# Kernel optimization log

Measured on AMD Instinct MI355X. Metric: run time of the kernel, lower is better.

The kernel has to match this reference:

```python
import jax, jax.numpy as jnp
import numpy as np

HEADS = 8
DIM = 512
SCALE = (DIM // HEADS) ** (-0.5)  # 0.125


def setup_inputs() -> dict:
    key = jax.random.key(0)
    k1, k2, k3, k4 = jax.random.split(key, 4)
    B, C, H, W = 4, DIM, 96, 96
    x = jax.random.normal(k1, (B, C, H, W), dtype=jnp.float32)
    # 1x1 conv weights collapsed to matrices [out_ch, in_ch]
    w_qkv = jax.random.normal(k2, (3 * DIM, DIM), dtype=jnp.float32) * (DIM ** -0.5)
    w_out = jax.random.normal(k3, (DIM, DIM), dtype=jnp.float32) * (DIM ** -0.5)
    b_out = jax.random.normal(k4, (DIM,), dtype=jnp.float32) * 0.01
    return {"x": x, "w_qkv": w_qkv, "w_out": w_out, "b_out": b_out}


def reference(x, w_qkv, w_out, b_out):
    # axis='height' branch of the original forward
    b, c, h, w = x.shape
    heads = HEADS
    d = c // heads
    # 1x1 conv == per-pixel GEMM: [B,3C,H,W]
    qkv = jnp.einsum('bchw,oc->bohw', x, w_qkv)
    # 'b (qkv heads d) x y -> qkv b heads x y d'
    qkv = qkv.reshape(b, 3, heads, d, h, w)
    qkv = jnp.transpose(qkv, (1, 0, 2, 4, 5, 3))  # [3, b, heads, h, w, d]
    q, k, v = qkv[0], qkv[1], qkv[2]
    # attention along the width axis, batched over (b, heads, row x)
    dots = jnp.einsum('bhxid,bhxjd->bhxij', q, k) * SCALE
    attn = jax.nn.softmax(dots, axis=-1)
    out = jnp.einsum('bhxij,bhxjd->bhxid', attn, v)  # [b, heads, h, w, d]
    # 'b heads x y d -> b (heads d) x y'
    out = jnp.transpose(out, (0, 1, 4, 2, 3)).reshape(b, heads * d, h, w)
    # to_out 1x1 conv with bias
    out = jnp.einsum('bchw,oc->bohw', out, w_out) + b_out[None, :, None, None]
    return out
```

## Files before the change

### kernel.cpp

```cpp
#include <hip/hip_runtime.h>

typedef unsigned short u16;
typedef unsigned int u32;
typedef __attribute__((ext_vector_type(8))) short short8;
typedef __attribute__((ext_vector_type(4))) float floatx4;

#define HEADS 8
#define DIM 512
#define HH 96
#define WW 96
#define NPIX 9216
#define M_TOT 36864
#define N_QKV 1536
#define SCALE 0.125f

__device__ __forceinline__ float b2f(u16 v){
    union{float f;u32 u;}x; x.u=((u32)v)<<16; return x.f;
}
__device__ __forceinline__ u16 f2b(float f){
    union{float f;u32 u;}x; x.f=f;
    u32 u=x.u + 0x7fffu + ((x.u>>16)&1u);
    return (u16)(u>>16);
}
__device__ __forceinline__ u32 pack2(float a,float b){
    return (u32)f2b(a) | ((u32)f2b(b)<<16);
}

__device__ __forceinline__ void gload16(const u16* g, u16* l){
    __builtin_amdgcn_global_load_lds(
        (const __attribute__((address_space(1))) u32*)g,
        (__attribute__((address_space(3))) u32*)l, 16, 0, 0);
}

__global__ void detect_dtype(const u16* __restrict__ wq, int* __restrict__ flag){
    __shared__ int cnt;
    if (threadIdx.x==0) cnt=0;
    __syncthreads();
    u16 u = wq[2*threadIdx.x];
    int e = (u>>7)&0xff;
    if (e>=100 && e<=128) atomicAdd(&cnt,1);
    __syncthreads();
    if (threadIdx.x==0) *flag = (cnt>128)?1:0;
}

__global__ __launch_bounds__(256)
void convert_w(const void* __restrict__ wq, const void* __restrict__ wo,
               const int* __restrict__ flag, u16* __restrict__ wqb, u16* __restrict__ wob){
    const int isb = *flag;
    int i = blockIdx.x*256 + threadIdx.x;
    const int nq = N_QKV*DIM;
    if (i < nq){
        wqb[i] = isb ? ((const u16*)wq)[i] : f2b(((const float*)wq)[i]);
    } else {
        int j = i - nq;
        wob[j] = isb ? ((const u16*)wo)[j] : f2b(((const float*)wo)[j]);
    }
}

__global__ __launch_bounds__(256)
void convert_x(const void* __restrict__ xv, const int* __restrict__ flag,
               u16* __restrict__ xb){
    __shared__ u16 tile[64][65];
    const int isb = *flag;
    const int p0 = blockIdx.x*64, c0 = blockIdx.y*64, b = blockIdx.z;
    const int t = threadIdx.x;
    const int pl = t&63, c4 = t>>6;
    const float* x32 = (const float*)xv;
    const u16*   x16 = (const u16*)xv;
    size_t src = ((size_t)b*DIM + c0 + c4)*NPIX + p0 + pl;
    #pragma unroll
    for (int i=0;i<16;i++){
        int cl = c4 + i*4;
        size_t s = src + (size_t)i*4*NPIX;
        tile[cl][pl] = isb ? x16[s] : f2b(x32[s]);
    }
    __syncthreads();
    const int cu = t&31, r8 = t>>5;
    u32* xb32 = (u32*)xb;
    #pragma unroll
    for (int i=0;i<8;i++){
        int pr = r8 + i*8;
        u32 v = (u32)tile[2*cu][pr] | ((u32)tile[2*cu+1][pr]<<16);
        xb32[((size_t)b*NPIX + p0 + pr)*(DIM/2) + (c0>>1) + cu] = v;
    }
}

__global__ __launch_bounds__(512, 2)
void gemm_qkv(const u16* __restrict__ A, const u16* __restrict__ B,
              u16* __restrict__ Cqk, u16* __restrict__ vt){
    __shared__ __align__(16) union ShMem {
        u16 tiles[65536];
        float ctQ[8][16][68];
        float ctV[8][16][132];
    } sh;
    u16* lds = sh.tiles;
    const int id = blockIdx.x;
    const int xcd = id & 7, slot = id >> 3;
    const int q6 = slot/6;
    const int by = xcd*18 + q6;
    const int bx = slot - q6*6;
    const int t = threadIdx.x;
    const int w = t>>6, l = t&63, lr = l&15, lq = l>>4;
    const int wm2 = w>>2, wn4 = w&3;
    const int m0 = by*256, n0 = bx*256;
    const u16* gA0 = A + (size_t)(m0 +       w*16 + lr)*DIM + lq*8;
    const u16* gA1 = A + (size_t)(m0 + 128 + w*16 + lr)*DIM + lq*8;
    const u16* gB0 = B + (size_t)(n0 +       w*16 + lr)*DIM + lq*8;
    const u16* gB1 = B + (size_t)(n0 + 128 + w*16 + lr)*DIM + lq*8;

#define STG(gp, opb, h, ko, bb) do { \
        const u16* _g = (gp) + (ko); \
        u16* _l = lds + (bb)*32768 + (opb) + ((h)*8 + w)*1024; \
        gload16(_g,      _l); \
        gload16(_g + 32, _l + 512); \
    } while(0)

    floatx4 acc[8][4] = {};
    STG(gA0, 0,     0, 0, 0);
    STG(gA1, 0,     1, 0, 0);
    STG(gB0, 16384, 0, 0, 0);
    STG(gB1, 16384, 1, 0, 0);

    #pragma unroll 1
    for (int ktile=0; ktile<8; ++ktile){
        const int cur = ktile&1, nxt = cur^1;
        const int ko = (ktile+1)*64;
        if (ktile < 7){
            STG(gA0, 0, 0, ko, nxt);
            asm volatile("s_waitcnt vmcnt(2)" ::: "memory");
        } else {
            asm volatile("s_waitcnt vmcnt(0)" ::: "memory");
        }
        __builtin_amdgcn_s_barrier();
        asm volatile("" ::: "memory");
        const u16* bA = lds + cur*32768 +         wm2*8192 + l*8;
        const u16* bB = lds + cur*32768 + 16384 + wn4*4096 + l*8;
        short8 af[4][2], bf[2][2];
        #pragma unroll
        for (int mi=0;mi<4;mi++){
            af[mi][0] = *(const short8*)(bA + mi*1024);
            af[mi][1] = *(const short8*)(bA + mi*1024 + 512);
        }
        #pragma unroll
        for (int ni=0;ni<2;ni++){
            bf[ni][0] = *(const short8*)(bB + ni*1024);
            bf[ni][1] = *(const short8*)(bB + ni*1024 + 512);
        }
        if (ktile < 7) STG(gA1, 0, 1, ko, nxt);
        __builtin_amdgcn_s_setprio(1);
        #pragma unroll
        for (int mi=0;mi<4;mi++)
            #pragma unroll
            for (int ni=0;ni<2;ni++){
                acc[mi][ni] = __builtin_amdgcn_mfma_f32_16x16x32_bf16(af[mi][0], bf[ni][0], acc[mi][ni], 0,0,0);
                acc[mi][ni] = __builtin_amdgcn_mfma_f32_16x16x32_bf16(af[mi][1], bf[ni][1], acc[mi][ni], 0,0,0);
            }
        __builtin_amdgcn_s_setprio(0);
        #pragma unroll
        for (int ni=0;ni<2;ni++){
            bf[ni][0] = *(const short8*)(bB + (2+ni)*1024);
            bf[ni][1] = *(const short8*)(bB + (2+ni)*1024 + 512);
        }
        if (ktile < 7) STG(gB0, 16384, 0, ko, nxt);
        __builtin_amdgcn_s_setprio(1);
        #pragma unroll
        for (int mi=0;mi<4;mi++)
            #pragma unroll
            for (int ni=0;ni<2;ni++){
                acc[mi][2+ni] = __builtin_amdgcn_mfma_f32_16x16x32_bf16(af[mi][0], bf[ni][0], acc[mi][2+ni], 0,0,0);
                acc[mi][2+ni] = __builtin_amdgcn_mfma_f32_16x16x32_bf16(af[mi][1], bf[ni][1], acc[mi][2+ni], 0,0,0);
            }
        __builtin_amdgcn_s_setprio(0);
        #pragma unroll
        for (int mi=0;mi<4;mi++){
            af[mi][0] = *(const short8*)(bA + (4+mi)*1024);
            af[mi][1] = *(const short8*)(bA + (4+mi)*1024 + 512);
        }
        if (ktile < 7) STG(gB1, 16384, 1, ko, nxt);
        __builtin_amdgcn_s_setprio(1);
        #pragma unroll
        for (int mi=0;mi<4;mi++)
            #pragma unroll
            for (int ni=0;ni<2;ni++){
                acc[4+mi][2+ni] = __builtin_amdgcn_mfma_f32_16x16x32_bf16(af[mi][0], bf[ni][0], acc[4+mi][2+ni], 0,0,0);
                acc[4+mi][2+ni] = __builtin_amdgcn_mfma_f32_16x16x32_bf16(af[mi][1], bf[ni][1], acc[4+mi][2+ni], 0,0,0);
            }
        __builtin_amdgcn_s_setprio(0);
        #pragma unroll
        for (int ni=0;ni<2;ni++){
            bf[ni][0] = *(const short8*)(bB + ni*1024);
            bf[ni][1] = *(const short8*)(bB + ni*1024 + 512);
        }
        __builtin_amdgcn_s_setprio(1);
        #pragma unroll
        for (int mi=0;mi<4;mi++)
            #pragma unroll
            for (int ni=0;ni<2;ni++){
                acc[4+mi][ni] = __builtin_amdgcn_mfma_f32_16x16x32_bf16(af[mi][0], bf[ni][0], acc[4+mi][ni], 0,0,0);
                acc[4+mi][ni] = __builtin_amdgcn_mfma_f32_16x16x32_bf16(af[mi][1], bf[ni][1], acc[4+mi][ni], 0,0,0);
            }
        __builtin_amdgcn_s_setprio(0);
        asm volatile("" ::: "memory");
        __builtin_amdgcn_s_barrier();
        asm volatile("" ::: "memory");
    }
#undef STG
    if (bx < 4){
        float (*ct)[68] = sh.ctQ[w];
        const int row = l>>2, cg = l&3;
        u16* dstbase = Cqk + (size_t)(m0 + wm2*128)*1024 + n0 + wn4*64 + cg*16;
        #pragma unroll
        for (int mi=0;mi<8;mi++){
            #pragma unroll
            for (int ni=0;ni<4;ni++)
                #pragma unroll
                for (int r=0;r<4;r++)
                    ct[lq*4+r][ni*16+lr] = acc[mi][ni][r];
            const float* cp = &ct[row][cg*16];
            float4 v0 = *(const float4*)(cp);
            float4 v1 = *(const float4*)(cp+4);
            float4 v2 = *(const float4*)(cp+8);
            float4 v3 = *(const float4*)(cp+12);
            uint4 s0, s1;
            s0.x=pack2(v0.x,v0.y); s0.y=pack2(v0.z,v0.w);
            s0.z=pack2(v1.x,v1.y); s0.w=pack2(v1.z,v1.w);
            s1.x=pack2(v2.x,v2.y); s1.y=pack2(v2.z,v2.w);
            s1.z=pack2(v3.x,v3.y); s1.w=pack2(v3.z,v3.w);
            u16* dst = dstbase + (size_t)(mi*16 + row)*1024;
            *((uint4*)dst)     = s0;
            *((uint4*)(dst+8)) = s1;
        }
    } else {
        float (*ct)[132] = sh.ctV[w];
        const int bat  = m0 / NPIX;
        const int pixb = m0 - bat*NPIX + wm2*128;
        const int nl = l>>2, seg = l&3;
        for (int ni=0; ni<4; ni++){
            #pragma unroll
            for (int mi=0;mi<8;mi++)
                #pragma unroll
                for (int r=0;r<4;r++)
                    ct[lr][mi*16 + lq*4 + r] = acc[mi][ni][r];
            int ch  = n0 + wn4*64 + ni*16 + nl - 1024;
            int bh2 = bat*8 + (ch>>6);
            int dd  = ch & 63;
            const float* cp = &ct[nl][seg*32];
            float4 v0 = *(const float4*)(cp);
            float4 v1 = *(const float4*)(cp+4);
            float4 v2 = *(const float4*)(cp+8);
            float4 v3 = *(const float4*)(cp+12);
            float4 v4 = *(const float4*)(cp+16);
            float4 v5 = *(const float4*)(cp+20);
            float4 v6 = *(const float4*)(cp+24);
            float4 v7 = *(const float4*)(cp+28);
            uint4 s0, s1, s2, s3;
            s0.x=pack2(v0.x,v0.y); s0.y=pack2(v0.z,v0.w);
            s0.z=pack2(v1.x,v1.y); s0.w=pack2(v1.z,v1.w);
            s1.x=pack2(v2.x,v2.y); s1.y=pack2(v2.z,v2.w);
            s1.z=pack2(v3.x,v3.y); s1.w=pack2(v3.z,v3.w);
            s2.x=pack2(v4.x,v4.y); s2.y=pack2(v4.z,v4.w);
            s2.z=pack2(v5.x,v5.y); s2.w=pack2(v5.z,v5.w);
            s3.x=pack2(v6.x,v6.y); s3.y=pack2(v6.z,v6.w);
            s3.z=pack2(v7.x,v7.y); s3.w=pack2(v7.z,v7.w);
            u16* dst = vt + (size_t)(bh2*64+dd)*NPIX + pixb + seg*32;
            *((uint4*)dst)      = s0;
            *((uint4*)(dst+8))  = s1;
            *((uint4*)(dst+16)) = s2;
            *((uint4*)(dst+24)) = s3;
        }
    }
}

__global__ __launch_bounds__(256)
void attn_kernel(const u16* __restrict__ qk, const u16* __restrict__ vt,
                 u16* __restrict__ attno){
    __shared__ __align__(16) u16 Qf[6144];
    __shared__ __align__(16) u16 Pb[9984];
    __shared__ float Ss[96][97];
    __shared__ float smax[96][2], ssum[96][2], rinv[96];
    const int t = threadIdx.x;
    const int w = t>>6, l = t&63, lr = l&15, lq = l>>4;
    const int wm = w&1, wn = w>>1;
    const int blk = blockIdx.x;
    const int row  = blk % HH;
    const int bh   = blk / HH;
    const int head = bh & 7;
    const int bat  = bh >> 3;
    const size_t pixrow = (size_t)bat*NPIX + row*WW;
    const u16* qbase = qk + pixrow*1024 + head*64;
    #pragma unroll
    for (int i=0;i<6;i++){
        int c  = w*6 + i;
        int c2 = (c<12) ? c : (c-12);
        int mt = c2>>1, ks = c2&1;
        const u16* g = qbase + (size_t)(mt*16+lr)*1024 + ks*32 + lq*8 + ((c<12)?0:512);
        u16* dst = ((c<12)?Qf:Pb) + c2*512 + l*8;
        gload16(g, dst);
    }
    __syncthreads();
    {
        floatx4 acc[3][3] = {};
        #pragma unroll
        for (int ks=0;ks<2;ks++){
            short8 af[3], bf[3];
            #pragma unroll
            for (int i=0;i<3;i++) af[i] = *(const short8*)&Qf[((wm*3+i)*2+ks)*512 + l*8];
            #pragma unroll
            for (int j=0;j<3;j++) bf[j] = *(const short8*)&Pb[((wn*3+j)*2+ks)*512 + l*8];
            #pragma unroll
            for (int i=0;i<3;i++)
                #pragma unroll
                for (int j=0;j<3;j++)
                    acc[i][j] = __builtin_amdgcn_mfma_f32_16x16x32_bf16(af[i], bf[j], acc[i][j], 0,0,0);
        }
        #pragma unroll
        for (int i=0;i<3;i++)
            #pragma unroll
            for (int j=0;j<3;j++)
                #pragma unroll
                for (int r=0;r<4;r++)
                    Ss[(wm*3+i)*16 + lq*4 + r][(wn*3+j)*16 + lr] = acc[i][j][r]*SCALE;
    }
    __syncthreads();
    #pragma unroll
    for (int i=0;i<3;i++){
        const u16* g = vt + (size_t)(bh*64 + w*16 + lr)*NPIX + row*WW + i*32 + lq*8;
        gload16(g, Qf + (w*3+i)*512 + l*8);
    }
    const int srow = t>>1, shalf = t&1, sbase = shalf*48;
    if (t < 192){
        float m = -1e30f;
        #pragma unroll 8
        for (int j=0;j<48;j++) m = fmaxf(m, Ss[srow][sbase+j]);
        smax[srow][shalf] = m;
    }
    __syncthreads();
    if (t < 192){
        float m2 = fmaxf(smax[srow][0], smax[srow][1]);
        float s = 0.f;
        u32* prow = (u32*)&Pb[srow*104 + sbase];
        #pragma unroll 8
        for (int j=0;j<48;j+=2){
            float e0 = __expf(Ss[srow][sbase+j]   - m2);
            float e1 = __expf(Ss[srow][sbase+j+1] - m2);
            prow[j>>1] = pack2(e0, e1);
            s += e0 + e1;
        }
        ssum[srow][shalf] = s;
    }
    __syncthreads();
    if (t < 192 && shalf==0) rinv[srow] = 1.f/(ssum[srow][0]+ssum[srow][1]);
    floatx4 o[3][2] = {};
    #pragma unroll
    for (int ks2=0;ks2<3;ks2++){
        short8 bf2[2];
        #pragma unroll
        for (int bb=0;bb<2;bb++)
            bf2[bb] = *(const short8*)&Qf[((wn*2+bb)*3+ks2)*512 + l*8];
        #pragma unroll
        for (int aa=0;aa<3;aa++){
            short8 af = *(const short8*)&Pb[((wm*3+aa)*16+lr)*104 + ks2*32 + lq*8];
            #pragma unroll
            for (int bb=0;bb<2;bb++)
                o[aa][bb] = __builtin_amdgcn_mfma_f32_16x16x32_bf16(af, bf2[bb], o[aa][bb], 0,0,0);
        }
    }
    __syncthreads();
    #pragma unroll
    for (int aa=0;aa<3;aa++){
        #pragma unroll
        for (int r=0;r<4;r++){
            int m = (wm*3+aa)*16 + lq*4 + r;
            float rv = rinv[m];
            int d0 = wn*32 + lr;
            Pb[m*72 + d0]      = f2b(o[aa][0][r]*rv);
            Pb[m*72 + d0 + 16] = f2b(o[aa][1][r]*rv);
        }
    }
    __syncthreads();
    #pragma unroll
    for (int i=0;i<3;i++){
        int idx = i*256 + t;
        int rr = idx>>3, seg = idx&7;
        uint4 vv = *(const uint4*)&Pb[rr*72 + seg*8];
        *(uint4*)(attno + (pixrow+rr)*512 + head*64 + seg*8) = vv;
    }
}

__global__ __launch_bounds__(512, 2)
void gemm_out(const u16* __restrict__ A, const u16* __restrict__ B,
              const void* __restrict__ bias, const int* __restrict__ flag,
              void* __restrict__ outv){
    __shared__ __align__(16) union ShMem {
        u16 tiles[65536];
        float ctV[8][16][132];
    } sh;
    u16* lds = sh.tiles;
    const int id = blockIdx.x;
    const int xcd = id & 7, slot = id >> 3;
    const int by = xcd*18 + (slot>>1);
    const int bx = slot & 1;
    const int t = threadIdx.x;
    const int w = t>>6, l = t&63, lr = l&15, lq = l>>4;
    const int wm2 = w>>2, wn4 = w&3;
    const int m0 = by*256, n0 = bx*256;
    const u16* gA0 = A + (size_t)(m0 +       w*16 + lr)*DIM + lq*8;
    const u16* gA1 = A + (size_t)(m0 + 128 + w*16 + lr)*DIM + lq*8;
    const u16* gB0 = B + (size_t)(n0 +       w*16 + lr)*DIM + lq*8;
    const u16* gB1 = B + (size_t)(n0 + 128 + w*16 + lr)*DIM + lq*8;

#define STG(gp, opb, h, ko, bb) do { \
        const u16* _g = (gp) + (ko); \
        u16* _l = lds + (bb)*32768 + (opb) + ((h)*8 + w)*1024; \
        gload16(_g,      _l); \
        gload16(_g + 32, _l + 512); \
    } while(0)

    floatx4 acc[8][4] = {};
    STG(gA0, 0,     0, 0, 0);
    STG(gA1, 0,     1, 0, 0);
    STG(gB0, 16384, 0, 0, 0);
    STG(gB1, 16384, 1, 0, 0);

    #pragma unroll 1
    for (int ktile=0; ktile<8; ++ktile){
        const int cur = ktile&1, nxt = cur^1;
        const int ko = (ktile+1)*64;
        if (ktile < 7){
            STG(gA0, 0, 0, ko, nxt);
            asm volatile("s_waitcnt vmcnt(2)" ::: "memory");
        } else {
            asm volatile("s_waitcnt vmcnt(0)" ::: "memory");
        }
        __builtin_amdgcn_s_barrier();
        asm volatile("" ::: "memory");
        const u16* bA = lds + cur*32768 +         wm2*8192 + l*8;
        const u16* bB = lds + cur*32768 + 16384 + wn4*4096 + l*8;
        short8 af[4][2], bf[2][2];
        #pragma unroll
        for (int mi=0;mi<4;mi++){
            af[mi][0] = *(const short8*)(bA + mi*1024);
            af[mi][1] = *(const short8*)(bA + mi*1024 + 512);
        }
        #pragma unroll
        for (int ni=0;ni<2;ni++){
            bf[ni][0] = *(const short8*)(bB + ni*1024);
            bf[ni][1] = *(const short8*)(bB + ni*1024 + 512);
        }
        if (ktile < 7) STG(gA1, 0, 1, ko, nxt);
        __builtin_amdgcn_s_setprio(1);
        #pragma unroll
        for (int mi=0;mi<4;mi++)
            #pragma unroll
            for (int ni=0;ni<2;ni++){
                acc[mi][ni] = __builtin_amdgcn_mfma_f32_16x16x32_bf16(af[mi][0], bf[ni][0], acc[mi][ni], 0,0,0);
                acc[mi][ni] = __builtin_amdgcn_mfma_f32_16x16x32_bf16(af[mi][1], bf[ni][1], acc[mi][ni], 0,0,0);
            }
        __builtin_amdgcn_s_setprio(0);
        #pragma unroll
        for (int ni=0;ni<2;ni++){
            bf[ni][0] = *(const short8*)(bB + (2+ni)*1024);
            bf[ni][1] = *(const short8*)(bB + (2+ni)*1024 + 512);
        }
        if (ktile < 7) STG(gB0, 16384, 0, ko, nxt);
        __builtin_amdgcn_s_setprio(1);
        #pragma unroll
        for (int mi=0;mi<4;mi++)
            #pragma unroll
            for (int ni=0;ni<2;ni++){
                acc[mi][2+ni] = __builtin_amdgcn_mfma_f32_16x16x32_bf16(af[mi][0], bf[ni][0], acc[mi][2+ni], 0,0,0);
                acc[mi][2+ni] = __builtin_amdgcn_mfma_f32_16x16x32_bf16(af[mi][1], bf[ni][1], acc[mi][2+ni], 0,0,0);
            }
        __builtin_amdgcn_s_setprio(0);
        #pragma unroll
        for (int mi=0;mi<4;mi++){
            af[mi][0] = *(const short8*)(bA + (4+mi)*1024);
            af[mi][1] = *(const short8*)(bA + (4+mi)*1024 + 512);
        }
        if (ktile < 7) STG(gB1, 16384, 1, ko, nxt);
        __builtin_amdgcn_s_setprio(1);
        #pragma unroll
        for (int mi=0;mi<4;mi++)
            #pragma unroll
            for (int ni=0;ni<2;ni++){
                acc[4+mi][2+ni] = __builtin_amdgcn_mfma_f32_16x16x32_bf16(af[mi][0], bf[ni][0], acc[4+mi][2+ni], 0,0,0);
                acc[4+mi][2+ni] = __builtin_amdgcn_mfma_f32_16x16x32_bf16(af[mi][1], bf[ni][1], acc[4+mi][2+ni], 0,0,0);
            }
        __builtin_amdgcn_s_setprio(0);
        #pragma unroll
        for (int ni=0;ni<2;ni++){
            bf[ni][0] = *(const short8*)(bB + ni*1024);
            bf[ni][1] = *(const short8*)(bB + ni*1024 + 512);
        }
        __builtin_amdgcn_s_setprio(1);
        #pragma unroll
        for (int mi=0;mi<4;mi++)
            #pragma unroll
            for (int ni=0;ni<2;ni++){
                acc[4+mi][ni] = __builtin_amdgcn_mfma_f32_16x16x32_bf16(af[mi][0], bf[ni][0], acc[4+mi][ni], 0,0,0);
                acc[4+mi][ni] = __builtin_amdgcn_mfma_f32_16x16x32_bf16(af[mi][1], bf[ni][1], acc[4+mi][ni], 0,0,0);
            }
        __builtin_amdgcn_s_setprio(0);
        asm volatile("" ::: "memory");
        __builtin_amdgcn_s_barrier();
        asm volatile("" ::: "memory");
    }
#undef STG
    const int isb = *flag;
    const int bat  = m0 / NPIX;
    const int pix0 = m0 - bat*NPIX + wm2*128;
    float (*ct)[132] = sh.ctV[w];
    const u16*   b16 = (const u16*)bias;
    const float* b32 = (const float*)bias;
    const int nl = l>>3, seg8 = l&7;
    for (int ni=0; ni<4; ni++){
        #pragma unroll
        for (int mi=0;mi<8;mi++)
            #pragma unroll
            for (int r=0;r<4;r++)
                ct[lr][mi*16 + lq*4 + r] = acc[mi][ni][r];
        #pragma unroll
        for (int p=0;p<2;p++){
            int nrow = nl + p*8;
            int ng = n0 + wn4*64 + ni*16 + nrow;
            float bv = isb ? b2f(b16[ng]) : b32[ng];
            const float* cp = &ct[nrow][seg8*16];
            float4 v0 = *(const float4*)(cp);
            float4 v1 = *(const float4*)(cp+4);
            float4 v2 = *(const float4*)(cp+8);
            float4 v3 = *(const float4*)(cp+12);
            v0.x+=bv; v0.y+=bv; v0.z+=bv; v0.w+=bv;
            v1.x+=bv; v1.y+=bv; v1.z+=bv; v1.w+=bv;
            v2.x+=bv; v2.y+=bv; v2.z+=bv; v2.w+=bv;
            v3.x+=bv; v3.y+=bv; v3.z+=bv; v3.w+=bv;
            size_t off = ((size_t)(bat*DIM + ng))*NPIX + pix0 + seg8*16;
            if (isb){
                uint4 s0, s1;
                s0.x=pack2(v0.x,v0.y); s0.y=pack2(v0.z,v0.w);
                s0.z=pack2(v1.x,v1.y); s0.w=pack2(v1.z,v1.w);
                s1.x=pack2(v2.x,v2.y); s1.y=pack2(v2.z,v2.w);
                s1.z=pack2(v3.x,v3.y); s1.w=pack2(v3.z,v3.w);
                *(uint4*)((u16*)outv + off)     = s0;
                *(uint4*)((u16*)outv + off + 8) = s1;
            } else {
                float* of = (float*)outv + off;
                *(float4*)(of)    = v0;
                *(float4*)(of+4)  = v1;
                *(float4*)(of+8)  = v2;
                *(float4*)(of+12) = v3;
            }
        }
    }
}

extern "C" void kernel_launch(void* const* d_in, const int* in_sizes, int n_in,
                              void* d_out, int out_size, void* d_ws, size_t ws_size,
                              hipStream_t stream){
    const void* x    = d_in[0];
    const void* wqkv = d_in[1];
    const void* wout = d_in[2];
    const void* bout = d_in[3];
    char* wsb = (char*)d_ws;
    int* flag    = (int*)wsb;
    u16* xb      = (u16*)(wsb + 256);
    u16* attn_ws = xb;
    u16* wqb     = xb + (size_t)M_TOT*DIM;
    u16* wob     = wqb + (size_t)N_QKV*DIM;
    u16* qk_ws   = wob + (size_t)DIM*DIM;
    u16* vt_ws   = qk_ws + (size_t)M_TOT*1024;
    detect_dtype<<<1, 256, 0, stream>>>((const u16*)wqkv, flag);
    convert_w<<<4096, 256, 0, stream>>>(wqkv, wout, flag, wqb, wob);
    convert_x<<<dim3(144, 8, 4), 256, 0, stream>>>(x, flag, xb);
    gemm_qkv<<<864, 512, 0, stream>>>(xb, wqb, qk_ws, vt_ws);
    attn_kernel<<<3072, 256, 0, stream>>>(qk_ws, vt_ws, attn_ws);
    gemm_out<<<288, 512, 0, stream>>>(attn_ws, wob, bout, flag, d_out);
}
```

Baseline: 347.2 us.

## Retile QKV and output GEMMs to 256x128 tiles with 4 waves, K-step 32

Both GEMM kernels go from 512-thread blocks with 256x256 output tiles and K-step 64 to 256-thread blocks with 256x128 tiles and K-step 32. LDS use drops from 128KB to 48KB, which doubles the number of blocks and should let more resident blocks overlap loads with MFMA. Each wave still computes a 128x64 sub-tile. The cost is more B-operand traffic per output, and twice as many barriers per K sweep. Separately, the bf16 pack helper now uses the hardware v_cvt_pk_bf16_f32 instruction in place of manual rounding.

```diff
diff --git a/kernel.cpp b/kernel.cpp
--- a/kernel.cpp
+++ b/kernel.cpp
@@ -23,7 +23,8 @@
     return (u16)(u>>16);
 }
 __device__ __forceinline__ u32 pack2(float a,float b){
-    return (u32)f2b(a) | ((u32)f2b(b)<<16);
+    u32 r; asm("v_cvt_pk_bf16_f32 %0, %1, %2" : "=v"(r) : "v"(a), "v"(b));
+    return r;
 }
 
 __device__ __forceinline__ void gload16(const u16* g, u16* l){
@@ -85,130 +86,100 @@
     }
 }
 
-__global__ __launch_bounds__(512, 2)
+__global__ __launch_bounds__(256, 2)
 void gemm_qkv(const u16* __restrict__ A, const u16* __restrict__ B,
               u16* __restrict__ Cqk, u16* __restrict__ vt){
     __shared__ __align__(16) union ShMem {
-        u16 tiles[65536];
-        float ctQ[8][16][68];
-        float ctV[8][16][132];
+        u16 tiles[24576];
+        float ctQ[4][16][68];
+        float ctV[4][16][132];
     } sh;
     u16* lds = sh.tiles;
     const int id = blockIdx.x;
     const int xcd = id & 7, slot = id >> 3;
-    const int q6 = slot/6;
-    const int by = xcd*18 + q6;
-    const int bx = slot - q6*6;
+    const int q12 = slot/12;
+    const int by = xcd*18 + q12;
+    const int bx = slot - q12*12;
     const int t = threadIdx.x;
     const int w = t>>6, l = t&63, lr = l&15, lq = l>>4;
-    const int wm2 = w>>2, wn4 = w&3;
-    const int m0 = by*256, n0 = bx*256;
-    const u16* gA0 = A + (size_t)(m0 +       w*16 + lr)*DIM + lq*8;
-    const u16* gA1 = A + (size_t)(m0 + 128 + w*16 + lr)*DIM + lq*8;
-    const u16* gB0 = B + (size_t)(n0 +       w*16 + lr)*DIM + lq*8;
-    const u16* gB1 = B + (size_t)(n0 + 128 + w*16 + lr)*DIM + lq*8;
-
-#define STG(gp, opb, h, ko, bb) do { \
-        const u16* _g = (gp) + (ko); \
-        u16* _l = lds + (bb)*32768 + (opb) + ((h)*8 + w)*1024; \
-        gload16(_g,      _l); \
-        gload16(_g + 32, _l + 512); \
-    } while(0)
+    const int wm2 = w>>1, wn2 = w&1;
+    const int m0 = by*256, n0 = bx*128;
+    const u16* gA = A + (size_t)(m0 + w*16 + lr)*DIM + lq*8;
+    const u16* gB = B + (size_t)(n0 + w*16 + lr)*DIM + lq*8;
+
+#define STG_A(h, ko, bb) gload16(gA + (size_t)(h)*32768 + (ko), \
+                                 lds + (bb)*12288 + ((h)*4 + w)*512)
+#define STG_B(h, ko, bb) gload16(gB + (size_t)(h)*32768 + (ko), \
+                                 lds + (bb)*12288 + 8192 + ((h)*4 + w)*512)
 
     floatx4 acc[8][4] = {};
-    STG(gA0, 0,     0, 0, 0);
-    STG(gA1, 0,     1, 0, 0);
-    STG(gB0, 16384, 0, 0, 0);
-    STG(gB1, 16384, 1, 0, 0);
+    STG_A(0,0,0); STG_A(1,0,0); STG_A(2,0,0); STG_A(3,0,0);
+    STG_B(0,0,0); STG_B(1,0,0);
 
     #pragma unroll 1
-    for (int ktile=0; ktile<8; ++ktile){
-        const int cur = ktile&1, nxt = cur^1;
-        const int ko = (ktile+1)*64;
-        if (ktile < 7){
-            STG(gA0, 0, 0, ko, nxt);
-            asm volatile("s_waitcnt vmcnt(2)" ::: "memory");
+    for (int kt=0; kt<16; ++kt){
+        const int cur = kt&1, nxt = cur^1;
+        const int ko = (kt+1)*32;
+        if (kt < 15){
+            STG_A(0, ko, nxt);
+            asm volatile("s_waitcnt vmcnt(1)" ::: "memory");
         } else {
             asm volatile("s_waitcnt vmcnt(0)" ::: "memory");
         }
         __builtin_amdgcn_s_barrier();
         asm volatile("" ::: "memory");
-        const u16* bA = lds + cur*32768 +         wm2*8192 + l*8;
-        const u16* bB = lds + cur*32768 + 16384 + wn4*4096 + l*8;
-        short8 af[4][2], bf[2][2];
-        #pragma unroll
-        for (int mi=0;mi<4;mi++){
-            af[mi][0] = *(const short8*)(bA + mi*1024);
-            af[mi][1] = *(const short8*)(bA + mi*1024 + 512);
-        }
-        #pragma unroll
-        for (int ni=0;ni<2;ni++){
-            bf[ni][0] = *(const short8*)(bB + ni*1024);
-            bf[ni][1] = *(const short8*)(bB + ni*1024 + 512);
-        }
-        if (ktile < 7) STG(gA1, 0, 1, ko, nxt);
-        __builtin_amdgcn_s_setprio(1);
-        #pragma unroll
-        for (int mi=0;mi<4;mi++)
-            #pragma unroll
-            for (int ni=0;ni<2;ni++){
-                acc[mi][ni] = __builtin_amdgcn_mfma_f32_16x16x32_bf16(af[mi][0], bf[ni][0], acc[mi][ni], 0,0,0);
-                acc[mi][ni] = __builtin_amdgcn_mfma_f32_16x16x32_bf16(af[mi][1], bf[ni][1], acc[mi][ni], 0,0,0);
-            }
-        __builtin_amdgcn_s_setprio(0);
-        #pragma unroll
-        for (int ni=0;ni<2;ni++){
-            bf[ni][0] = *(const short8*)(bB + (2+ni)*1024);
-            bf[ni][1] = *(const short8*)(bB + (2+ni)*1024 + 512);
-        }
-        if (ktile < 7) STG(gB0, 16384, 0, ko, nxt);
-        __builtin_amdgcn_s_setprio(1);
-        #pragma unroll
-        for (int mi=0;mi<4;mi++)
-            #pragma unroll
-            for (int ni=0;ni<2;ni++){
-                acc[mi][2+ni] = __builtin_amdgcn_mfma_f32_16x16x32_bf16(af[mi][0], bf[ni][0], acc[mi][2+ni], 0,0,0);
-                acc[mi][2+ni] = __builtin_amdgcn_mfma_f32_16x16x32_bf16(af[mi][1], bf[ni][1], acc[mi][2+ni], 0,0,0);
-            }
-        __builtin_amdgcn_s_setprio(0);
-        #pragma unroll
-        for (int mi=0;mi<4;mi++){
-            af[mi][0] = *(const short8*)(bA + (4+mi)*1024);
-            af[mi][1] = *(const short8*)(bA + (4+mi)*1024 + 512);
-        }
-        if (ktile < 7) STG(gB1, 16384, 1, ko, nxt);
-        __builtin_amdgcn_s_setprio(1);
-        #pragma unroll
-        for (int mi=0;mi<4;mi++)
-            #pragma unroll
-            for (int ni=0;ni<2;ni++){
-                acc[4+mi][2+ni] = __builtin_amdgcn_mfma_f32_16x16x32_bf16(af[mi][0], bf[ni][0], acc[4+mi][2+ni], 0,0,0);
-                acc[4+mi][2+ni] = __builtin_amdgcn_mfma_f32_16x16x32_bf16(af[mi][1], bf[ni][1], acc[4+mi][2+ni], 0,0,0);
-            }
-        __builtin_amdgcn_s_setprio(0);
-        #pragma unroll
-        for (int ni=0;ni<2;ni++){
-            bf[ni][0] = *(const short8*)(bB + ni*1024);
-            bf[ni][1] = *(const short8*)(bB + ni*1024 + 512);
-        }
-        __builtin_amdgcn_s_setprio(1);
-        #pragma unroll
-        for (int mi=0;mi<4;mi++)
-            #pragma unroll
-            for (int ni=0;ni<2;ni++){
-                acc[4+mi][ni] = __builtin_amdgcn_mfma_f32_16x16x32_bf16(af[mi][0], bf[ni][0], acc[4+mi][ni], 0,0,0);
-                acc[4+mi][ni] = __builtin_amdgcn_mfma_f32_16x16x32_bf16(af[mi][1], bf[ni][1], acc[4+mi][ni], 0,0,0);
-            }
+        const u16* bA = lds + cur*12288 +        wm2*4096 + l*8;
+        const u16* bB = lds + cur*12288 + 8192 + wn2*2048 + l*8;
+        short8 af[4], blo[2], bhi[2];
+        #pragma unroll
+        for (int mi=0;mi<4;mi++) af[mi] = *(const short8*)(bA + mi*512);
+        blo[0] = *(const short8*)(bB);
+        blo[1] = *(const short8*)(bB + 512);
+        if (kt < 15){ STG_A(1, ko, nxt); STG_A(2, ko, nxt); }
+        __builtin_amdgcn_s_setprio(1);
+        #pragma unroll
+        for (int mi=0;mi<4;mi++){
+            acc[mi][0] = __builtin_amdgcn_mfma_f32_16x16x32_bf16(af[mi], blo[0], acc[mi][0], 0,0,0);
+            acc[mi][1] = __builtin_amdgcn_mfma_f32_16x16x32_bf16(af[mi], blo[1], acc[mi][1], 0,0,0);
+        }
+        __builtin_amdgcn_s_setprio(0);
+        bhi[0] = *(const short8*)(bB + 1024);
+        bhi[1] = *(const short8*)(bB + 1536);
+        if (kt < 15){ STG_A(3, ko, nxt); STG_B(0, ko, nxt); }
+        __builtin_amdgcn_s_setprio(1);
+        #pragma unroll
+        for (int mi=0;mi<4;mi++){
+            acc[mi][2] = __builtin_amdgcn_mfma_f32_16x16x32_bf16(af[mi], bhi[0], acc[mi][2], 0,0,0);
+            acc[mi][3] = __builtin_amdgcn_mfma_f32_16x16x32_bf16(af[mi], bhi[1], acc[mi][3], 0,0,0);
+        }
+        __builtin_amdgcn_s_setprio(0);
+        #pragma unroll
+        for (int mi=0;mi<4;mi++) af[mi] = *(const short8*)(bA + 2048 + mi*512);
+        if (kt < 15){ STG_B(1, ko, nxt); }
+        __builtin_amdgcn_s_setprio(1);
+        #pragma unroll
+        for (int mi=0;mi<4;mi++){
+            acc[4+mi][2] = __builtin_amdgcn_mfma_f32_16x16x32_bf16(af[mi], bhi[0], acc[4+mi][2], 0,0,0);
+            acc[4+mi][3] = __builtin_amdgcn_mfma_f32_16x16x32_bf16(af[mi], bhi[1], acc[4+mi][3], 0,0,0);
+        }
+        __builtin_amdgcn_s_setprio(0);
+        __builtin_amdgcn_s_setprio(1);
+        #pragma unroll
+        for (int mi=0;mi<4;mi++){
+            acc[4+mi][0] = __builtin_amdgcn_mfma_f32_16x16x32_bf16(af[mi], blo[0], acc[4+mi][0], 0,0,0);
+            acc[4+mi][1] = __builtin_amdgcn_mfma_f32_16x16x32_bf16(af[mi], blo[1], acc[4+mi][1], 0,0,0);
+        }
         __builtin_amdgcn_s_setprio(0);
         asm volatile("" ::: "memory");
         __builtin_amdgcn_s_barrier();
         asm volatile("" ::: "memory");
     }
-#undef STG
-    if (bx < 4){
+#undef STG_A
+#undef STG_B
+    if (bx < 8){
         float (*ct)[68] = sh.ctQ[w];
         const int row = l>>2, cg = l&3;
-        u16* dstbase = Cqk + (size_t)(m0 + wm2*128)*1024 + n0 + wn4*64 + cg*16;
+        u16* dstbase = Cqk + (size_t)(m0 + wm2*128)*1024 + n0 + wn2*64 + cg*16;
         #pragma unroll
         for (int mi=0;mi<8;mi++){
             #pragma unroll
@@ -241,7 +212,7 @@
                 #pragma unroll
                 for (int r=0;r<4;r++)
                     ct[lr][mi*16 + lq*4 + r] = acc[mi][ni][r];
-            int ch  = n0 + wn4*64 + ni*16 + nl - 1024;
+            int ch  = n0 + wn2*64 + ni*16 + nl - 1024;
             int bh2 = bat*8 + (ch>>6);
             int dd  = ch & 63;
             const float* cp = &ct[nl][seg*32];
@@ -387,125 +358,95 @@
     }
 }
 
-__global__ __launch_bounds__(512, 2)
+__global__ __launch_bounds__(256, 2)
 void gemm_out(const u16* __restrict__ A, const u16* __restrict__ B,
               const void* __restrict__ bias, const int* __restrict__ flag,
               void* __restrict__ outv){
     __shared__ __align__(16) union ShMem {
-        u16 tiles[65536];
-        float ctV[8][16][132];
+        u16 tiles[24576];
+        float ctV[4][16][132];
     } sh;
     u16* lds = sh.tiles;
     const int id = blockIdx.x;
     const int xcd = id & 7, slot = id >> 3;
-    const int by = xcd*18 + (slot>>1);
-    const int bx = slot & 1;
+    const int by = xcd*18 + (slot>>2);
+    const int bx = slot & 3;
     const int t = threadIdx.x;
     const int w = t>>6, l = t&63, lr = l&15, lq = l>>4;
-    const int wm2 = w>>2, wn4 = w&3;
-    const int m0 = by*256, n0 = bx*256;
-    const u16* gA0 = A + (size_t)(m0 +       w*16 + lr)*DIM + lq*8;
-    const u16* gA1 = A + (size_t)(m0 + 128 + w*16 + lr)*DIM + lq*8;
-    const u16* gB0 = B + (size_t)(n0 +       w*16 + lr)*DIM + lq*8;
-    const u16* gB1 = B + (size_t)(n0 + 128 + w*16 + lr)*DIM + lq*8;
-
-#define STG(gp, opb, h, ko, bb) do { \
-        const u16* _g = (gp) + (ko); \
-        u16* _l = lds + (bb)*32768 + (opb) + ((h)*8 + w)*1024; \
-        gload16(_g,      _l); \
-        gload16(_g + 32, _l + 512); \
-    } while(0)
+    const int wm2 = w>>1, wn2 = w&1;
+    const int m0 = by*256, n0 = bx*128;
+    const u16* gA = A + (size_t)(m0 + w*16 + lr)*DIM + lq*8;
+    const u16* gB = B + (size_t)(n0 + w*16 + lr)*DIM + lq*8;
+
+#define STG_A(h, ko, bb) gload16(gA + (size_t)(h)*32768 + (ko), \
+                                 lds + (bb)*12288 + ((h)*4 + w)*512)
+#define STG_B(h, ko, bb) gload16(gB + (size_t)(h)*32768 + (ko), \
+                                 lds + (bb)*12288 + 8192 + ((h)*4 + w)*512)
 
     floatx4 acc[8][4] = {};
-    STG(gA0, 0,     0, 0, 0);
-    STG(gA1, 0,     1, 0, 0);
-    STG(gB0, 16384, 0, 0, 0);
-    STG(gB1, 16384, 1, 0, 0);
+    STG_A(0,0,0); STG_A(1,0,0); STG_A(2,0,0); STG_A(3,0,0);
+    STG_B(0,0,0); STG_B(1,0,0);
 
     #pragma unroll 1
-    for (int ktile=0; ktile<8; ++ktile){
-        const int cur = ktile&1, nxt = cur^1;
-        const int ko = (ktile+1)*64;
-        if (ktile < 7){
-            STG(gA0, 0, 0, ko, nxt);
-            asm volatile("s_waitcnt vmcnt(2)" ::: "memory");
+    for (int kt=0; kt<16; ++kt){
+        const int cur = kt&1, nxt = cur^1;
+        const int ko = (kt+1)*32;
+        if (kt < 15){
+            STG_A(0, ko, nxt);
+            asm volatile("s_waitcnt vmcnt(1)" ::: "memory");
         } else {
             asm volatile("s_waitcnt vmcnt(0)" ::: "memory");
         }
         __builtin_amdgcn_s_barrier();
         asm volatile("" ::: "memory");
-        const u16* bA = lds + cur*32768 +         wm2*8192 + l*8;
-        const u16* bB = lds + cur*32768 + 16384 + wn4*4096 + l*8;
-        short8 af[4][2], bf[2][2];
-        #pragma unroll
-        for (int mi=0;mi<4;mi++){
-            af[mi][0] = *(const short8*)(bA + mi*1024);
-            af[mi][1] = *(const short8*)(bA + mi*1024 + 512);
-        }
-        #pragma unroll
-        for (int ni=0;ni<2;ni++){
-            bf[ni][0] = *(const short8*)(bB + ni*1024);
-            bf[ni][1] = *(const short8*)(bB + ni*1024 + 512);
-        }
-        if (ktile < 7) STG(gA1, 0, 1, ko, nxt);
-        __builtin_amdgcn_s_setprio(1);
-        #pragma unroll
-        for (int mi=0;mi<4;mi++)
-            #pragma unroll
-            for (int ni=0;ni<2;ni++){
-                acc[mi][ni] = __builtin_amdgcn_mfma_f32_16x16x32_bf16(af[mi][0], bf[ni][0], acc[mi][ni], 0,0,0);
-                acc[mi][ni] = __builtin_amdgcn_mfma_f32_16x16x32_bf16(af[mi][1], bf[ni][1], acc[mi][ni], 0,0,0);
-            }
-        __builtin_amdgcn_s_setprio(0);
-        #pragma unroll
-        for (int ni=0;ni<2;ni++){
-            bf[ni][0] = *(const short8*)(bB + (2+ni)*1024);
-            bf[ni][1] = *(const short8*)(bB + (2+ni)*1024 + 512);
-        }
-        if (ktile < 7) STG(gB0, 16384, 0, ko, nxt);
-        __builtin_amdgcn_s_setprio(1);
-        #pragma unroll
-        for (int mi=0;mi<4;mi++)
-            #pragma unroll
-            for (int ni=0;ni<2;ni++){
-                acc[mi][2+ni] = __builtin_amdgcn_mfma_f32_16x16x32_bf16(af[mi][0], bf[ni][0], acc[mi][2+ni], 0,0,0);
-                acc[mi][2+ni] = __builtin_amdgcn_mfma_f32_16x16x32_bf16(af[mi][1], bf[ni][1], acc[mi][2+ni], 0,0,0);
-            }
-        __builtin_amdgcn_s_setprio(0);
-        #pragma unroll
-        for (int mi=0;mi<4;mi++){
-            af[mi][0] = *(const short8*)(bA + (4+mi)*1024);
-            af[mi][1] = *(const short8*)(bA + (4+mi)*1024 + 512);
-        }
-        if (ktile < 7) STG(gB1, 16384, 1, ko, nxt);
-        __builtin_amdgcn_s_setprio(1);
-        #pragma unroll
-        for (int mi=0;mi<4;mi++)
-            #pragma unroll
-            for (int ni=0;ni<2;ni++){
-                acc[4+mi][2+ni] = __builtin_amdgcn_mfma_f32_16x16x32_bf16(af[mi][0], bf[ni][0], acc[4+mi][2+ni], 0,0,0);
-                acc[4+mi][2+ni] = __builtin_amdgcn_mfma_f32_16x16x32_bf16(af[mi][1], bf[ni][1], acc[4+mi][2+ni], 0,0,0);
-            }
-        __builtin_amdgcn_s_setprio(0);
-        #pragma unroll
-        for (int ni=0;ni<2;ni++){
-            bf[ni][0] = *(const short8*)(bB + ni*1024);
-            bf[ni][1] = *(const short8*)(bB + ni*1024 + 512);
-        }
-        __builtin_amdgcn_s_setprio(1);
-        #pragma unroll
-        for (int mi=0;mi<4;mi++)
-            #pragma unroll
-            for (int ni=0;ni<2;ni++){
-                acc[4+mi][ni] = __builtin_amdgcn_mfma_f32_16x16x32_bf16(af[mi][0], bf[ni][0], acc[4+mi][ni], 0,0,0);
-                acc[4+mi][ni] = __builtin_amdgcn_mfma_f32_16x16x32_bf16(af[mi][1], bf[ni][1], acc[4+mi][ni], 0,0,0);
-            }
+        const u16* bA = lds + cur*12288 +        wm2*4096 + l*8;
+        const u16* bB = lds + cur*12288 + 8192 + wn2*2048 + l*8;
+        short8 af[4], blo[2], bhi[2];
+        #pragma unroll
+        for (int mi=0;mi<4;mi++) af[mi] = *(const short8*)(bA + mi*512);
+        blo[0] = *(const short8*)(bB);
+        blo[1] = *(const short8*)(bB + 512);
+        if (kt < 15){ STG_A(1, ko, nxt); STG_A(2, ko, nxt); }
+        __builtin_amdgcn_s_setprio(1);
+        #pragma unroll
+        for (int mi=0;mi<4;mi++){
+            acc[mi][0] = __builtin_amdgcn_mfma_f32_16x16x32_bf16(af[mi], blo[0], acc[mi][0], 0,0,0);
+            acc[mi][1] = __builtin_amdgcn_mfma_f32_16x16x32_bf16(af[mi], blo[1], acc[mi][1], 0,0,0);
+        }
+        __builtin_amdgcn_s_setprio(0);
+        bhi[0] = *(const short8*)(bB + 1024);
+        bhi[1] = *(const short8*)(bB + 1536);
+        if (kt < 15){ STG_A(3, ko, nxt); STG_B(0, ko, nxt); }
+        __builtin_amdgcn_s_setprio(1);
+        #pragma unroll
+        for (int mi=0;mi<4;mi++){
+            acc[mi][2] = __builtin_amdgcn_mfma_f32_16x16x32_bf16(af[mi], bhi[0], acc[mi][2], 0,0,0);
+            acc[mi][3] = __builtin_amdgcn_mfma_f32_16x16x32_bf16(af[mi], bhi[1], acc[mi][3], 0,0,0);
+        }
+        __builtin_amdgcn_s_setprio(0);
+        #pragma unroll
+        for (int mi=0;mi<4;mi++) af[mi] = *(const short8*)(bA + 2048 + mi*512);
+        if (kt < 15){ STG_B(1, ko, nxt); }
+        __builtin_amdgcn_s_setprio(1);
+        #pragma unroll
+        for (int mi=0;mi<4;mi++){
+            acc[4+mi][2] = __builtin_amdgcn_mfma_f32_16x16x32_bf16(af[mi], bhi[0], acc[4+mi][2], 0,0,0);
+            acc[4+mi][3] = __builtin_amdgcn_mfma_f32_16x16x32_bf16(af[mi], bhi[1], acc[4+mi][3], 0,0,0);
+        }
+        __builtin_amdgcn_s_setprio(0);
+        __builtin_amdgcn_s_setprio(1);
+        #pragma unroll
+        for (int mi=0;mi<4;mi++){
+            acc[4+mi][0] = __builtin_amdgcn_mfma_f32_16x16x32_bf16(af[mi], blo[0], acc[4+mi][0], 0,0,0);
+            acc[4+mi][1] = __builtin_amdgcn_mfma_f32_16x16x32_bf16(af[mi], blo[1], acc[4+mi][1], 0,0,0);
+        }
         __builtin_amdgcn_s_setprio(0);
         asm volatile("" ::: "memory");
         __builtin_amdgcn_s_barrier();
         asm volatile("" ::: "memory");
     }
-#undef STG
+#undef STG_A
+#undef STG_B
     const int isb = *flag;
     const int bat  = m0 / NPIX;
     const int pix0 = m0 - bat*NPIX + wm2*128;
@@ -522,7 +463,7 @@
         #pragma unroll
         for (int p=0;p<2;p++){
             int nrow = nl + p*8;
-            int ng = n0 + wn4*64 + ni*16 + nrow;
+            int ng = n0 + wn2*64 + ni*16 + nrow;
             float bv = isb ? b2f(b16[ng]) : b32[ng];
             const float* cp = &ct[nrow][seg8*16];
             float4 v0 = *(const float4*)(cp);
@@ -571,7 +512,7 @@
     detect_dtype<<<1, 256, 0, stream>>>((const u16*)wqkv, flag);
     convert_w<<<4096, 256, 0, stream>>>(wqkv, wout, flag, wqb, wob);
     convert_x<<<dim3(144, 8, 4), 256, 0, stream>>>(x, flag, xb);
-    gemm_qkv<<<864, 512, 0, stream>>>(xb, wqb, qk_ws, vt_ws);
+    gemm_qkv<<<1728, 256, 0, stream>>>(xb, wqb, qk_ws, vt_ws);
     attn_kernel<<<3072, 256, 0, stream>>>(qk_ws, vt_ws, attn_ws);
-    gemm_out<<<288, 512, 0, stream>>>(attn_ws, wob, bout, flag, d_out);
-}
+    gemm_out<<<576, 256, 0, stream>>>(attn_ws, wob, bout, flag, d_out);
+}
```

After: 364.2 us. 4.9% more time.
